# Optimization experiments

Measured on AMD Instinct MI355X. Metric: run time of the kernel, lower is better.

## Reference

```python
import jax, jax.numpy as jnp
import numpy as np
from jax import lax

T, B, IN, H, L, C = 1024, 2048, 2, 20, 6, 2


def setup_inputs() -> dict:
    key = jax.random.key(0)
    ks = jax.random.split(key, 8)
    s = 1.0 / np.sqrt(H)  # PyTorch RNN init scale (uniform bound); use scaled normals
    return {
        "x": jax.random.normal(ks[0], (T, B, IN), jnp.float32),
        "W_ih0": jax.random.normal(ks[1], (H, IN), jnp.float32) * s,
        "W_ih": jax.random.normal(ks[2], (L - 1, H, H), jnp.float32) * s,
        "W_hh": jax.random.normal(ks[3], (L, H, H), jnp.float32) * s,
        "b_ih": jax.random.normal(ks[4], (L, H), jnp.float32) * s,
        "b_hh": jax.random.normal(ks[5], (L, H), jnp.float32) * s,
        "fc_w": jax.random.normal(ks[6], (C, H), jnp.float32) * s,
        "fc_b": jax.random.normal(ks[7], (C,), jnp.float32) * s,
    }


def _rnn_layer(x, Wih, Whh, bih, bhh):
    # x: [T, B, in_dim]; h_t = relu(x_t @ Wih^T + b_ih + h_{t-1} @ Whh^T + b_hh)
    xb = jnp.einsum('tbi,hi->tbh', x, Wih) + (bih + bhh)  # precompute input projection
    h0 = jnp.zeros((x.shape[1], Whh.shape[0]), x.dtype)

    def step(h, xt):
        h = jax.nn.relu(xt + h @ Whh.T)
        return h, h

    _, out = lax.scan(step, h0, xb)
    return out  # [T, B, H]


def reference(x, W_ih0, W_ih, W_hh, b_ih, b_hh, fc_w, fc_b):
    out = _rnn_layer(x, W_ih0, W_hh[0], b_ih[0], b_hh[0])
    for l in range(1, L):
        out = _rnn_layer(out, W_ih[l - 1], W_hh[l], b_ih[l], b_hh[l])
    logits = jnp.einsum('tbh,ch->tbc', out, fc_w) + fc_b
    return jax.nn.log_softmax(logits, axis=2)
```

## Files before the change

### kernel.cpp

```cpp
#include <hip/hip_runtime.h>
#include <math.h>


#define TT 1024
#define BB 2048
#define HH 20
#define LL 6
#define SLOTW 40
#define BUFW  (8 * SLOTW)
#define XS 0

#define WS_WI   0
#define WS_BIAS 2400

typedef float f4 __attribute__((ext_vector_type(4)));

__global__ void stage_ws(const float* __restrict__ Wih0,
                         const float* __restrict__ Wih,
                         const float* __restrict__ bih,
                         const float* __restrict__ bhh,
                         const float* __restrict__ fcb,
                         float* __restrict__ ws) {
    const int i = threadIdx.x + blockIdx.x * blockDim.x;
    if (i < 2400) {
        const int l = i / 400, r = i % 400, j = r / 20, k = r % 20;
        float v;
        if (l == 0) v = (k < 2) ? Wih0[j * 2 + k] : 0.f;
        else        v = Wih[(l - 1) * 400 + r];
        ws[WS_WI + i] = v;
    }
    if (i < 122) {
        const int role = i >> 1, c = i & 1;
        float v;
        if (role < 60) {
            const int l = role / 10, j = 2 * (role % 10) + c;
            v = bih[l * HH + j] + bhh[l * HH + j];
        } else {
            v = fcb[c];
        }
        ws[WS_BIAS + i] = v;
    }
}

__global__ void logsm(float* __restrict__ o) {
    const size_t n = (size_t)TT * BB;
    float2* p = (float2*)o;
    for (size_t idx = (size_t)blockIdx.x * blockDim.x + threadIdx.x; idx < n;
         idx += (size_t)gridDim.x * blockDim.x) {
        float2 v = p[idx];
        const float mx  = fmaxf(v.x, v.y);
        const float lse = mx + __logf(__expf(v.x - mx) + __expf(v.y - mx));
        p[idx] = make_float2(v.x - lse, v.y - lse);
    }
}


#define MAC4(acc, W, Q) do {                                       \
    acc = fmaf((W).x, (Q).x, acc); acc = fmaf((W).y, (Q).y, acc);  \
    acc = fmaf((W).z, (Q).z, acc); acc = fmaf((W).w, (Q).w, acc); } while (0)

#define MICRO(M_, C0,C1,C2,C3,C4, N0,N1,N2,N3,N4, ST_) do {                        \
    float* const wb_ = (((M_) & 1) ? bufB : bufA);                                 \
    const float* const rb_ = (((M_) & 1) ? bufA : bufB);                           \
    { const f4* jp_ = (const f4*)(rb_ + ioff);                                     \
      N0 = jp_[0]; N1 = jp_[1]; N2 = jp_[2]; N3 = jp_[3]; N4 = jp_[4]; }           \
    float ai0 = bt.x, ai1 = bt.y, ah0 = 0.f, ah1 = 0.f;                            \
    MAC4(ai0, wiA0, C0); MAC4(ai1, wiB0, C0);                                      \
    MAC4(ai0, wiA1, C1); MAC4(ai1, wiB1, C1);                                      \
    MAC4(ai0, wiA2, C2); MAC4(ai1, wiB2, C2);                                      \
    MAC4(ai0, wiA3, C3); MAC4(ai1, wiB3, C3);                                      \
    MAC4(ai0, wiA4, C4); MAC4(ai1, wiB4, C4);                                      \
    MAC4(ah0, whA0, rq0); MAC4(ah1, whB0, rq0);                                    \
    MAC4(ah0, whA1, rq1); MAC4(ah1, whB1, rq1);                                    \
    MAC4(ah0, whA2, rq2); MAC4(ah1, whB2, rq2);                                    \
    MAC4(ah0, whA3, rq3); MAC4(ah1, whB3, rq3);                                    \
    MAC4(ah0, whA4, rq4); MAC4(ah1, whB4, rq4);                                    \
    const float a0 = ah0 + ai0;                                                    \
    const float a1 = ah1 + ai1;                                                    \
    if (lane < 60) {                                                               \
        if ((ST_) || (unsigned)((M_) - lag2) < TT)                                 \
            *(float2*)(wb_ + hoff + j) = make_float2(fmaxf(a0, 0.f), fmaxf(a1, 0.f)); \
    } else if (lane == 60) {                                                       \
        if ((ST_) || (unsigned)((M_) - 12) < TT) *oph = make_float2(a0, a1);       \
        oph += BB;                                                                 \
    } else {                                                                       \
        if (rdc == ((M_) % 3)) {                                                   \
            if ((ST_) || (M_) + 2 < TT) *(float2*)(wb_ + XS) = xh;                 \
            if ((ST_)) xh = *xq; else if (xq <= xend) xh = *xq;                    \
            xq += 3 * (size_t)BB;                                                  \
        }                                                                          \
    }                                                                              \
    { const f4* hp_ = (const f4*)(wb_ + hoff);                                     \
      rq0 = hp_[0]; rq1 = hp_[1]; rq2 = hp_[2]; rq3 = hp_[3]; rq4 = hp_[4]; }      \
    __builtin_amdgcn_sched_barrier(0);                                             \
} while (0)

#define MPAIR(M_, ST_)                                                             \
    MICRO((M_),     iq0,iq1,iq2,iq3,iq4, jq0,jq1,jq2,jq3,jq4, ST_);                \
    MICRO((M_) + 1, jq0,jq1,jq2,jq3,jq4, iq0,iq1,iq2,iq3,iq4, ST_)

__global__ __attribute__((amdgpu_flat_work_group_size(64, 64), amdgpu_waves_per_eu(2, 2)))
void rnn_fused(const float* __restrict__ x,
               const float* __restrict__ Whh,
               const float* __restrict__ fcw,
               const float* __restrict__ ws,
               float* __restrict__ out)
{
    __shared__ __align__(16) float As[2 * BUFW];

    const int lane = threadIdx.x;
    const int b = ((blockIdx.x & 7) << 8) | (blockIdx.x >> 3);

    const int  role = (lane < 60) ? lane : 60;
    const int  l    = role / 10;
    const int  j    = 2 * (role % 10);
    const bool head = (role == 60);
    const int  lag2 = 2 * l;

    const f4* pwh = (const f4*)(head ? Whh : (Whh + (l * HH + j) * HH));
    const f4* pwi = (const f4*)(head ? fcw : (ws + WS_WI + (l * HH + j) * HH));
    const float2 bt = *(const float2*)(ws + WS_BIAS + 2 * role);

    f4 whA0 = pwh[0], whA1 = pwh[1], whA2 = pwh[2], whA3 = pwh[3], whA4 = pwh[4];
    f4 whB0 = pwh[5], whB1 = pwh[6], whB2 = pwh[7], whB3 = pwh[8], whB4 = pwh[9];
    f4 wiA0 = pwi[0], wiA1 = pwi[1], wiA2 = pwi[2], wiA3 = pwi[3], wiA4 = pwi[4];
    f4 wiB0 = pwi[5], wiB1 = pwi[6], wiB2 = pwi[7], wiB3 = pwi[8], wiB4 = pwi[9];

    const int ioff = l * SLOTW;
    const int hoff = (l + 1) * SLOTW;

    float* const bufA = As;
    float* const bufB = As + BUFW;

    for (int i = lane; i < 2 * BUFW; i += 64) As[i] = 0.f;
    const float2* xp = (const float2*)x;
    float2 xh = make_float2(0.f, 0.f);
    if (lane == 61) *(float2*)(bufA + XS) = xp[b];
    if (lane == 62) *(float2*)(bufB + XS) = xp[(size_t)BB + b];
    if (lane >= 61) xh = xp[(size_t)(lane - 61 + 2) * BB + b];

    const int rdc = (lane >= 61) ? (lane - 61) : 0;
    const float2* xq   = xp + (size_t)(rdc + 5) * BB + b;
    const float2* xend = xp + (size_t)(TT - 1) * BB + b;
    float2* oph = (float2*)out + b - (ptrdiff_t)12 * BB;

    f4 iq0, iq1, iq2, iq3, iq4, jq0, jq1, jq2, jq3, jq4;
    f4 rq0, rq1, rq2, rq3, rq4;
    { const f4* ip_ = (const f4*)(bufA + ioff);
      iq0 = ip_[0]; iq1 = ip_[1]; iq2 = ip_[2]; iq3 = ip_[3]; iq4 = ip_[4]; }
    { const f4* hp_ = (const f4*)(bufB + hoff);
      rq0 = hp_[0]; rq1 = hp_[1]; rq2 = hp_[2]; rq3 = hp_[3]; rq4 = hp_[4]; }

    MPAIR(0, 0);  MPAIR(2, 0);  MPAIR(4, 0);
    MPAIR(6, 0);  MPAIR(8, 0);  MPAIR(10, 0);

#pragma unroll 1
    for (int it = 0; it < 167; ++it) {
        MPAIR(12, 1); MPAIR(14, 1); MPAIR(16, 1);
    }

    MPAIR(1014, 0); MPAIR(1016, 0); MPAIR(1018, 0); MPAIR(1020, 0);
    MPAIR(1022, 0); MPAIR(1024, 0); MPAIR(1026, 0); MPAIR(1028, 0);
    MPAIR(1030, 0); MPAIR(1032, 0); MPAIR(1034, 0);
}

extern "C" void kernel_launch(void* const* d_in, const int* in_sizes, int n_in,
                              void* d_out, int out_size, void* d_ws, size_t ws_size,
                              hipStream_t stream) {
    const float* x    = (const float*)d_in[0];
    const float* Wih0 = (const float*)d_in[1];
    const float* Wih  = (const float*)d_in[2];
    const float* Whh  = (const float*)d_in[3];
    const float* bih  = (const float*)d_in[4];
    const float* bhh  = (const float*)d_in[5];
    const float* fcw  = (const float*)d_in[6];
    const float* fcb  = (const float*)d_in[7];
    float* out = (float*)d_out;
    float* ws  = (float*)d_ws;

    stage_ws<<<dim3(3), dim3(1024), 0, stream>>>(Wih0, Wih, bih, bhh, fcb, ws);
    rnn_fused<<<dim3(BB), dim3(64), 0, stream>>>(x, Whh, fcw, ws, out);
    logsm<<<dim3(2048), dim3(256), 0, stream>>>(out);
}
```

Before: 429.6 us.

## Process two batch elements per wave with interleaved independent recurrences

Each 64-lane block now handles two batch columns at once, halving the grid to 1024 blocks. Every step runs two independent dot-product chains per lane, which gives more instruction-level parallelism in place of the earlier cross-step register prefetch pipelining. x and output are loaded and stored as float4, and LDS doubles to hold both columns. Occupancy drops to one wave per EU, trading wave-level parallelism for ILP. The layer wavefront lag changes from two micro-steps per layer to one.

```diff
diff --git a/kernel.cpp b/kernel.cpp
--- a/kernel.cpp
+++ b/kernel.cpp
@@ -9,6 +9,7 @@
 #define SLOTW 40
 #define BUFW  (8 * SLOTW)
 #define XS 0
+#define NB4 1024
 
 #define WS_WI   0
 #define WS_BIAS 2400
@@ -59,63 +60,67 @@
     acc = fmaf((W).x, (Q).x, acc); acc = fmaf((W).y, (Q).y, acc);  \
     acc = fmaf((W).z, (Q).z, acc); acc = fmaf((W).w, (Q).w, acc); } while (0)
 
-#define MICRO(M_, C0,C1,C2,C3,C4, N0,N1,N2,N3,N4, ST_) do {                        \
-    float* const wb_ = (((M_) & 1) ? bufB : bufA);                                 \
-    const float* const rb_ = (((M_) & 1) ? bufA : bufB);                           \
-    { const f4* jp_ = (const f4*)(rb_ + ioff);                                     \
-      N0 = jp_[0]; N1 = jp_[1]; N2 = jp_[2]; N3 = jp_[3]; N4 = jp_[4]; }           \
-    float ai0 = bt.x, ai1 = bt.y, ah0 = 0.f, ah1 = 0.f;                            \
-    MAC4(ai0, wiA0, C0); MAC4(ai1, wiB0, C0);                                      \
-    MAC4(ai0, wiA1, C1); MAC4(ai1, wiB1, C1);                                      \
-    MAC4(ai0, wiA2, C2); MAC4(ai1, wiB2, C2);                                      \
-    MAC4(ai0, wiA3, C3); MAC4(ai1, wiB3, C3);                                      \
-    MAC4(ai0, wiA4, C4); MAC4(ai1, wiB4, C4);                                      \
-    MAC4(ah0, whA0, rq0); MAC4(ah1, whB0, rq0);                                    \
-    MAC4(ah0, whA1, rq1); MAC4(ah1, whB1, rq1);                                    \
-    MAC4(ah0, whA2, rq2); MAC4(ah1, whB2, rq2);                                    \
-    MAC4(ah0, whA3, rq3); MAC4(ah1, whB3, rq3);                                    \
-    MAC4(ah0, whA4, rq4); MAC4(ah1, whB4, rq4);                                    \
-    const float a0 = ah0 + ai0;                                                    \
-    const float a1 = ah1 + ai1;                                                    \
+#define MACS(P0,P1,Q0,Q1, H0,H1,H2,H3,H4, I0,I1,I2,I3,I4)          \
+    MAC4(P0,whA0,H0); MAC4(P1,whB0,H0); MAC4(Q0,wiA0,I0); MAC4(Q1,wiB0,I0); \
+    MAC4(P0,whA1,H1); MAC4(P1,whB1,H1); MAC4(Q0,wiA1,I1); MAC4(Q1,wiB1,I1); \
+    MAC4(P0,whA2,H2); MAC4(P1,whB2,H2); MAC4(Q0,wiA2,I2); MAC4(Q1,wiB2,I2); \
+    MAC4(P0,whA3,H3); MAC4(P1,whB3,H3); MAC4(Q0,wiA3,I3); MAC4(Q1,wiB3,I3); \
+    MAC4(P0,whA4,H4); MAC4(P1,whB4,H4); MAC4(Q0,wiA4,I4); MAC4(Q1,wiB4,I4)
+
+#define STEP(S_, PH_, RB_, WB_, ST_, FF_) do {                                     \
+    const float* rb0_ = (RB_);              float* wb0_ = (WB_);                   \
+    const float* rb1_ = rb0_ + 2 * BUFW;    float* wb1_ = wb0_ + 2 * BUFW;         \
+    const f4* hp0_ = (const f4*)(rb0_ + hoff); const f4* ip0_ = (const f4*)(rb0_ + ioff); \
+    const f4* hp1_ = (const f4*)(rb1_ + hoff); const f4* ip1_ = (const f4*)(rb1_ + ioff); \
+    const f4 h00=hp0_[0],h01=hp0_[1],h02=hp0_[2],h03=hp0_[3],h04=hp0_[4];          \
+    const f4 i00=ip0_[0],i01=ip0_[1],i02=ip0_[2],i03=ip0_[3],i04=ip0_[4];          \
+    const f4 h10=hp1_[0],h11=hp1_[1],h12=hp1_[2],h13=hp1_[3],h14=hp1_[4];          \
+    const f4 i10=ip1_[0],i11=ip1_[1],i12=ip1_[2],i13=ip1_[3],i14=ip1_[4];          \
+    float p0=0.f,p1=0.f,q0=bt.x,q1=bt.y;                                           \
+    float r0=0.f,r1=0.f,s0=bt.x,s1=bt.y;                                           \
+    MACS(p0,p1,q0,q1, h00,h01,h02,h03,h04, i00,i01,i02,i03,i04);                   \
+    MACS(r0,r1,s0,s1, h10,h11,h12,h13,h14, i10,i11,i12,i13,i14);                   \
+    const float a00 = p0 + q0, a01 = p1 + q1;                                      \
+    const float a10 = r0 + s0, a11 = r1 + s1;                                      \
     if (lane < 60) {                                                               \
-        if ((ST_) || (unsigned)((M_) - lag2) < TT)                                 \
-            *(float2*)(wb_ + hoff + j) = make_float2(fmaxf(a0, 0.f), fmaxf(a1, 0.f)); \
+        if ((ST_) || (unsigned)((S_) - l) < TT) {                                  \
+            *(float2*)(wb0_ + hoff + j) = make_float2(fmaxf(a00,0.f), fmaxf(a01,0.f)); \
+            *(float2*)(wb1_ + hoff + j) = make_float2(fmaxf(a10,0.f), fmaxf(a11,0.f)); \
+        }                                                                          \
     } else if (lane == 60) {                                                       \
-        if ((ST_) || (unsigned)((M_) - 12) < TT) *oph = make_float2(a0, a1);       \
-        oph += BB;                                                                 \
+        if ((ST_) || (S_) >= LL) { f4 o_; o_.x=a00; o_.y=a01; o_.z=a10; o_.w=a11;  \
+                                   *oph4 = o_; }                                   \
+        oph4 += NB4;                                                               \
     } else {                                                                       \
-        if (rdc == ((M_) % 3)) {                                                   \
-            if ((ST_) || (M_) + 2 < TT) *(float2*)(wb_ + XS) = xh;                 \
-            if ((ST_)) xh = *xq; else if (xq <= xend) xh = *xq;                    \
-            xq += 3 * (size_t)BB;                                                  \
+        if (rdc == (PH_)) {                                                        \
+            if ((ST_) || (S_) + 1 < TT) {                                          \
+                *(float2*)(wb0_ + XS) = make_float2(xh.x, xh.y);                   \
+                *(float2*)(wb1_ + XS) = make_float2(xh.z, xh.w);                   \
+            }                                                                      \
+            if ((ST_)) xh = *xq4; else if (xq4 <= xend4) xh = *xq4;                \
+            xq4 += 3 * (size_t)NB4;                                                \
         }                                                                          \
     }                                                                              \
-    { const f4* hp_ = (const f4*)(wb_ + hoff);                                     \
-      rq0 = hp_[0]; rq1 = hp_[1]; rq2 = hp_[2]; rq3 = hp_[3]; rq4 = hp_[4]; }      \
-    __builtin_amdgcn_sched_barrier(0);                                             \
+    if (FF_) __builtin_amdgcn_sched_barrier(0);                                    \
+    else     __builtin_amdgcn_sched_barrier(0x77);   \
 } while (0)
 
-#define MPAIR(M_, ST_)                                                             \
-    MICRO((M_),     iq0,iq1,iq2,iq3,iq4, jq0,jq1,jq2,jq3,jq4, ST_);                \
-    MICRO((M_) + 1, jq0,jq1,jq2,jq3,jq4, iq0,iq1,iq2,iq3,iq4, ST_)
-
-__global__ __attribute__((amdgpu_flat_work_group_size(64, 64), amdgpu_waves_per_eu(2, 2)))
+__global__ __attribute__((amdgpu_flat_work_group_size(64, 64), amdgpu_waves_per_eu(1, 1)))
 void rnn_fused(const float* __restrict__ x,
                const float* __restrict__ Whh,
                const float* __restrict__ fcw,
                const float* __restrict__ ws,
                float* __restrict__ out)
 {
-    __shared__ __align__(16) float As[2 * BUFW];
+    __shared__ __align__(16) float As[4 * BUFW];
 
     const int lane = threadIdx.x;
-    const int b = ((blockIdx.x & 7) << 8) | (blockIdx.x >> 3);
+    const int bq = ((blockIdx.x & 7) << 7) | (blockIdx.x >> 3);
 
     const int  role = (lane < 60) ? lane : 60;
     const int  l    = role / 10;
     const int  j    = 2 * (role % 10);
     const bool head = (role == 60);
-    const int  lag2 = 2 * l;
 
     const f4* pwh = (const f4*)(head ? Whh : (Whh + (l * HH + j) * HH));
     const f4* pwi = (const f4*)(head ? fcw : (ws + WS_WI + (l * HH + j) * HH));
@@ -132,36 +137,36 @@
     float* const bufA = As;
     float* const bufB = As + BUFW;
 
-    for (int i = lane; i < 2 * BUFW; i += 64) As[i] = 0.f;
-    const float2* xp = (const float2*)x;
-    float2 xh = make_float2(0.f, 0.f);
-    if (lane == 61) *(float2*)(bufA + XS) = xp[b];
-    if (lane == 62) *(float2*)(bufB + XS) = xp[(size_t)BB + b];
-    if (lane >= 61) xh = xp[(size_t)(lane - 61 + 2) * BB + b];
+    for (int i = lane; i < 4 * BUFW; i += 64) As[i] = 0.f;
+
+    const f4* xp4 = (const f4*)x;
+    f4 xh; xh.x = 0.f; xh.y = 0.f; xh.z = 0.f; xh.w = 0.f;
+    if (lane == 61) { const f4 v = xp4[bq];
+                      *(float2*)(bufA + XS)            = make_float2(v.x, v.y);
+                      *(float2*)(bufA + 2*BUFW + XS)   = make_float2(v.z, v.w); }
+    if (lane >= 61) xh = xp4[(size_t)(lane - 60) * NB4 + bq];
 
     const int rdc = (lane >= 61) ? (lane - 61) : 0;
-    const float2* xq   = xp + (size_t)(rdc + 5) * BB + b;
-    const float2* xend = xp + (size_t)(TT - 1) * BB + b;
-    float2* oph = (float2*)out + b - (ptrdiff_t)12 * BB;
+    const f4* xq4   = xp4 + (size_t)(rdc + 4) * NB4 + bq;
+    const f4* xend4 = xp4 + (size_t)(TT - 1) * NB4 + bq;
+    f4* oph4 = (f4*)out + bq - (ptrdiff_t)LL * NB4;
 
-    f4 iq0, iq1, iq2, iq3, iq4, jq0, jq1, jq2, jq3, jq4;
-    f4 rq0, rq1, rq2, rq3, rq4;
-    { const f4* ip_ = (const f4*)(bufA + ioff);
-      iq0 = ip_[0]; iq1 = ip_[1]; iq2 = ip_[2]; iq3 = ip_[3]; iq4 = ip_[4]; }
-    { const f4* hp_ = (const f4*)(bufB + hoff);
-      rq0 = hp_[0]; rq1 = hp_[1]; rq2 = hp_[2]; rq3 = hp_[3]; rq4 = hp_[4]; }
-
-    MPAIR(0, 0);  MPAIR(2, 0);  MPAIR(4, 0);
-    MPAIR(6, 0);  MPAIR(8, 0);  MPAIR(10, 0);
+    STEP(0, 0, bufA, bufB, 0, 1); STEP(1, 1, bufB, bufA, 0, 1);
+    STEP(2, 2, bufA, bufB, 0, 1); STEP(3, 0, bufB, bufA, 0, 1);
+    STEP(4, 1, bufA, bufB, 0, 1); STEP(5, 2, bufB, bufA, 0, 1);
 
 #pragma unroll 1
-    for (int it = 0; it < 167; ++it) {
-        MPAIR(12, 1); MPAIR(14, 1); MPAIR(16, 1);
+    for (int it = 0; it < 169; ++it) {
+        STEP(0, 0, bufA, bufB, 1, 0); STEP(0, 1, bufB, bufA, 1, 0);
+        STEP(0, 2, bufA, bufB, 1, 0); STEP(0, 0, bufB, bufA, 1, 0);
+        STEP(0, 1, bufA, bufB, 1, 0); STEP(0, 2, bufB, bufA, 1, 0);
     }
 
-    MPAIR(1014, 0); MPAIR(1016, 0); MPAIR(1018, 0); MPAIR(1020, 0);
-    MPAIR(1022, 0); MPAIR(1024, 0); MPAIR(1026, 0); MPAIR(1028, 0);
-    MPAIR(1030, 0); MPAIR(1032, 0); MPAIR(1034, 0);
+    STEP(1020, 0, bufA, bufB, 0, 1); STEP(1021, 1, bufB, bufA, 0, 1);
+    STEP(1022, 2, bufA, bufB, 0, 1); STEP(1023, 0, bufB, bufA, 0, 1);
+    STEP(1024, 1, bufA, bufB, 0, 1); STEP(1025, 2, bufB, bufA, 0, 1);
+    STEP(1026, 0, bufA, bufB, 0, 1); STEP(1027, 1, bufB, bufA, 0, 1);
+    STEP(1028, 2, bufA, bufB, 0, 1); STEP(1029, 0, bufB, bufA, 0, 1);
 }
 
 extern "C" void kernel_launch(void* const* d_in, const int* in_sizes, int n_in,
@@ -179,6 +184,6 @@
     float* ws  = (float*)d_ws;
 
     stage_ws<<<dim3(3), dim3(1024), 0, stream>>>(Wih0, Wih, bih, bhh, fcb, ws);
-    rnn_fused<<<dim3(BB), dim3(64), 0, stream>>>(x, Whh, fcw, ws, out);
+    rnn_fused<<<dim3(1024), dim3(64), 0, stream>>>(x, Whh, fcw, ws, out);
     logsm<<<dim3(2048), dim3(256), 0, stream>>>(out);
 }
```

Measured after the change: 485.6 us. 13.0% more time.
